# Performance work log

Hardware: AMD Instinct MI355X
Metric: run time of the kernel (lower is better)

## Reference

```python
import jax, jax.numpy as jnp
import numpy as np

N = 500000   # candidates
C = 128      # field centers
D = 64       # latent dim
EPS = 1e-6
TEMP = 0.1
DT = 0.1


def setup_inputs() -> dict:
    key = jax.random.key(0)
    k1, k2, k3, k4 = jax.random.split(key, 4)
    query_z = jax.random.normal(k1, (1, D), dtype=jnp.float32)
    candidate_z = jax.random.normal(k2, (N, D), dtype=jnp.float32)
    centers = jax.random.normal(k3, (C, D), dtype=jnp.float32)
    mus = jax.random.uniform(k4, (C,), dtype=jnp.float32) * 0.5 + 0.1  # positive masses
    return {"query_z": query_z, "candidate_z": candidate_z, "centers": centers, "mus": mus}


def _cdist(a, b):
    # Euclidean distance matrix (|a|^2 + |b|^2 - 2 a.b)^(1/2), clamped for stability
    d2 = (jnp.sum(a * a, axis=-1, keepdims=True)
          + jnp.sum(b * b, axis=-1)[None, :]
          - 2.0 * (a @ b.T))
    return jnp.sqrt(jnp.maximum(d2, 1e-12))


def _potential(z, centers, mus):
    # pot_i = sum_j mu_j / (dist(z_i, c_j) + eps)   -> (len(z),)
    d = _cdist(z, centers)                      # (B, C)
    return jnp.sum(mus[None, :] / (d + EPS), axis=1)


def _pm_field(z, centers, mus):
    # Gravitational flow step: z + dt * sum_j mu_j * (c_j - z) / (r^3 + eps)
    diff = centers[None, :, :] - z[:, None, :]          # (B, C, D)
    r = jnp.sqrt(jnp.maximum(jnp.sum(diff * diff, axis=-1, keepdims=True), 1e-12))
    return z + DT * jnp.sum(mus[None, :, None] * diff / (r ** 3 + EPS), axis=1)


def reference(query_z, candidate_z, centers, mus):
    query_output = _pm_field(query_z, centers, mus)        # (1, D)
    q_pot = _potential(query_z, centers, mus)              # (1,)
    c_pot = _potential(candidate_z, centers, mus)          # (N,)
    logits = -jnp.abs(q_pot - c_pot) / TEMP                # (N,)
    attention = jax.nn.softmax(logits, axis=0)             # (N,)
    return query_output, attention
```

## Files before the change

### kernel.cpp

```cpp
#include <hip/hip_runtime.h>
#include <hip/hip_bf16.h>

#define N_CAND     500000
#define N_PAIRS    15625
#define IT_LOG2E   14.426950408889634f
#define DT_STEP    0.1f
#define POT_BLOCKS 1024
#define STRIDE     (POT_BLOCKS * 4)

typedef __attribute__((ext_vector_type(8))) short  short8;
typedef __attribute__((ext_vector_type(4))) float  floatx4;
typedef __attribute__((ext_vector_type(4))) unsigned int uintx4;

__device__ inline unsigned pk(float lo, float hi) {
    return __builtin_amdgcn_perm(__builtin_bit_cast(unsigned, hi),
                                 __builtin_bit_cast(unsigned, lo), 0x07060302u);
}

__device__ inline short8 pack8(floatx4 v0, floatx4 v1, float& ss) {
    uintx4 w;
    w[0] = pk(v0[0], v0[1]); w[1] = pk(v0[2], v0[3]);
    w[2] = pk(v1[0], v1[1]); w[3] = pk(v1[2], v1[3]);
#pragma unroll
    for (int k = 0; k < 4; ++k) {
        ss = fmaf(v0[k], v0[k], ss);
        ss = fmaf(v1[k], v1[k], ss);
    }
    return __builtin_bit_cast(short8, w);
}

__global__ __attribute__((amdgpu_waves_per_eu(2, 4))) __launch_bounds__(256)
void pot_kernel(const float* __restrict__ qz, const float* __restrict__ cand,
                const float* __restrict__ centers, const float* __restrict__ mus,
                float* __restrict__ out, float* __restrict__ partials) {
    __shared__ __align__(16) short8  cfrag[18][2][64];
    __shared__ __align__(16) floatx4 ncin[8][4];
    __shared__ __align__(16) floatx4 muv8[8][4];
    __shared__ float qred[4], sred[4], wj[128];

    int tid = threadIdx.x, wid = tid >> 6, lane = tid & 63;
    int lr = lane & 15;
    int lg = lane >> 4;

    {
        int j = tid >> 1;
        int h = tid & 1;
        const float* crow = centers + j * 64 + h * 32;
        const float* qrow = qz + h * 32;
        float ssd = 0.f;
#pragma unroll
        for (int k = 0; k < 8; ++k) {
            floatx4 c4 = *(const floatx4*)(crow + k * 4);
            floatx4 q4 = *(const floatx4*)(qrow + k * 4);
#pragma unroll
            for (int x = 0; x < 4; ++x) { float df = c4[x] - q4[x]; ssd = fmaf(df, df, ssd); }
        }
        ssd += __shfl_xor(ssd, 1);
        float rs = __builtin_amdgcn_rsqf(fmaxf(ssd, 1e-12f));
        float mu_j = mus[j];
        float potj = (h == 0) ? mu_j * rs : 0.f;
        if (blockIdx.x == 0 && h == 0)
            wj[j] = mu_j * rs * rs * rs;
#pragma unroll
        for (int m = 1; m < 64; m <<= 1) potj += __shfl_xor(potj, m);
        if (lane == 0) qred[wid] = potj;
    }

#pragma unroll
    for (int c2 = 0; c2 < 2; ++c2) {
        int ct = wid * 2 + c2;
        int j = ct * 16 + lr;
        const float* p = centers + j * 64 + lg * 8;
        float ncp = 0.f;
        short8 b0 = pack8(*(const floatx4*)p,        *(const floatx4*)(p + 4),  ncp);
        short8 b1 = pack8(*(const floatx4*)(p + 32), *(const floatx4*)(p + 36), ncp);
        cfrag[ct][0][lane] = b0;
        cfrag[ct][1][lane] = b1;
        ncp += __shfl_xor(ncp, 16);
        ncp += __shfl_xor(ncp, 32);
        if (lg == 0) ((float*)ncin)[ct * 16 + lr] = -0.5f * ncp;
        if (lg == 1) ((float*)muv8)[ct * 16 + lr] = mus[j];
    }
    __syncthreads();
    float q_pot = qred[0] + qred[1] + qred[2] + qred[3];

    if (blockIdx.x == 0 && tid < 64) {
        float qd = qz[tid];
        float acc = 0.f;
        for (int jj = 0; jj < 128; ++jj)
            acc = fmaf(wj[jj], centers[jj * 64 + tid] - qd, acc);
        out[tid] = fmaf(DT_STEP, acc, qd);
    }

    float lsum = 0.f;
    const float* baseA = cand + (size_t)lr * 64 + lg * 8;
    floatx4 v0, v1, v2, v3, v4, v5, v6, v7;
#define LOADP(pp) { const float* pa = baseA + (size_t)(pp) * 2048;          \
        v0 = *(const floatx4*)pa;        v1 = *(const floatx4*)(pa + 4);    \
        v2 = *(const floatx4*)(pa + 32); v3 = *(const floatx4*)(pa + 36);   \
        const float* pb = pa + 1024;                                        \
        v4 = *(const floatx4*)pb;        v5 = *(const floatx4*)(pb + 4);    \
        v6 = *(const floatx4*)(pb + 32); v7 = *(const floatx4*)(pb + 36); }

    int p = blockIdx.x * 4 + wid;
    LOADP(p);
    while (p < N_PAIRS) {
        float nzA = 0.f, nzB = 0.f;
        short8 afA0 = pack8(v0, v1, nzA), afA1 = pack8(v2, v3, nzA);
        short8 afB0 = pack8(v4, v5, nzB), afB1 = pack8(v6, v7, nzB);
        size_t r0 = (size_t)p * 32;
        p += STRIDE;
        if (p < N_PAIRS) LOADP(p);

        nzA += __shfl_xor(nzA, 16); nzA += __shfl_xor(nzA, 32);
        nzB += __shfl_xor(nzB, 16); nzB += __shfl_xor(nzB, 32);

        float potA = 0.f, potB = 0.f;
#pragma unroll
        for (int ct = 0; ct < 8; ++ct) {
            floatx4 nci = ncin[ct][lg];
            floatx4 m4  = muv8[ct][lg];
            short8 f0 = cfrag[ct][0][lane];
            short8 f1 = cfrag[ct][1][lane];
            floatx4 aA = __builtin_amdgcn_mfma_f32_16x16x32_bf16(f0, afA0, nci, 0, 0, 0);
            aA         = __builtin_amdgcn_mfma_f32_16x16x32_bf16(f1, afA1, aA,  0, 0, 0);
            floatx4 aB = __builtin_amdgcn_mfma_f32_16x16x32_bf16(f0, afB0, nci, 0, 0, 0);
            aB         = __builtin_amdgcn_mfma_f32_16x16x32_bf16(f1, afB1, aB,  0, 0, 0);
#pragma unroll
            for (int r = 0; r < 4; ++r) {
                potA = fmaf(m4[r], __builtin_amdgcn_rsqf(fmaf(-2.f, aA[r], nzA)), potA);
                potB = fmaf(m4[r], __builtin_amdgcn_rsqf(fmaf(-2.f, aB[r], nzB)), potB);
            }
        }
        potA += __shfl_xor(potA, 16); potA += __shfl_xor(potA, 32);
        potB += __shfl_xor(potB, 16); potB += __shfl_xor(potB, 32);

        if (lg == 0) {
            float eA = exp2f(-IT_LOG2E * fabsf(q_pot - potA));
            float eB = exp2f(-IT_LOG2E * fabsf(q_pot - potB));
            out[64 + r0 + lr]      = eA;
            out[64 + r0 + 16 + lr] = eB;
            lsum += eA + eB;
        }
    }
#undef LOADP

#pragma unroll
    for (int m = 1; m < 64; m <<= 1) lsum += __shfl_xor(lsum, m);
    if (lane == 0) sred[wid] = lsum;
    __syncthreads();
    if (tid == 0) partials[blockIdx.x] = sred[0] + sred[1] + sred[2] + sred[3];
}

__global__ __launch_bounds__(256)
void norm_kernel(float* __restrict__ att, const float* __restrict__ partials) {
    int tid = threadIdx.x;
    float p = partials[tid] + partials[tid + 256] + partials[tid + 512] + partials[tid + 768];
#pragma unroll
    for (int m = 1; m < 64; m <<= 1) p += __shfl_xor(p, m);
    __shared__ float red[4];
    if ((tid & 63) == 0) red[tid >> 6] = p;
    __syncthreads();
    float inv = 1.0f / (red[0] + red[1] + red[2] + red[3]);
    int i = blockIdx.x * 256 + tid;
    if (i < N_CAND / 4) {
        floatx4 v = *(floatx4*)(att + (size_t)i * 4);
#pragma unroll
        for (int k = 0; k < 4; ++k) v[k] *= inv;
        *(floatx4*)(att + (size_t)i * 4) = v;
    }
}

extern "C" void kernel_launch(void* const* d_in, const int* in_sizes, int n_in,
                              void* d_out, int out_size, void* d_ws, size_t ws_size,
                              hipStream_t stream) {
    const float* qz   = (const float*)d_in[0];
    const float* cand = (const float*)d_in[1];
    const float* ctr  = (const float*)d_in[2];
    const float* mus  = (const float*)d_in[3];
    float* out = (float*)d_out;
    float* ws  = (float*)d_ws;

    pot_kernel<<<POT_BLOCKS, 256, 0, stream>>>(qz, cand, ctr, mus, out, ws + 256);
    int blocks2 = (N_CAND / 4 + 255) / 256;
    norm_kernel<<<blocks2, 256, 0, stream>>>(out + 64, ws + 256);
}
```

Baseline: 39.84 us.

## Raise occupancy target, drop manual prefetch, hoist center constants into registers

Raises the waves-per-EU minimum from 2 to 3 and removes the software double-buffered candidate prefetch, relying on extra resident waves to hide global load latency instead. The per-center-tile bias and mass vectors now live in registers rather than being re-read from LDS on every iteration. The exp/store epilogue is split across two lane groups so each lane handles one value instead of one group doing both. The main risk is register pressure from the 64 hoisted floats against the tighter VGPR budget, which could cause spills or fail to reach the extra occupancy, and losing the explicit prefetch may expose load latency.

Result: slower. 53.90 us (+35.3%).

```diff
diff --git a/kernel.cpp b/kernel.cpp
--- a/kernel.cpp
+++ b/kernel.cpp
@@ -29,7 +29,7 @@
     return __builtin_bit_cast(short8, w);
 }
 
-__global__ __attribute__((amdgpu_waves_per_eu(2, 4))) __launch_bounds__(256)
+__global__ __attribute__((amdgpu_waves_per_eu(3, 4))) __launch_bounds__(256)
 void pot_kernel(const float* __restrict__ qz, const float* __restrict__ cand,
                 const float* __restrict__ centers, const float* __restrict__ mus,
                 float* __restrict__ out, float* __restrict__ partials) {
@@ -92,58 +92,55 @@
         out[tid] = fmaf(DT_STEP, acc, qd);
     }
 
+    floatx4 ncr[8], mur[8];
+#pragma unroll
+    for (int ct = 0; ct < 8; ++ct) { ncr[ct] = ncin[ct][lg]; mur[ct] = muv8[ct][lg]; }
+
     float lsum = 0.f;
     const float* baseA = cand + (size_t)lr * 64 + lg * 8;
-    floatx4 v0, v1, v2, v3, v4, v5, v6, v7;
-#define LOADP(pp) { const float* pa = baseA + (size_t)(pp) * 2048;          \
-        v0 = *(const floatx4*)pa;        v1 = *(const floatx4*)(pa + 4);    \
-        v2 = *(const floatx4*)(pa + 32); v3 = *(const floatx4*)(pa + 36);   \
-        const float* pb = pa + 1024;                                        \
-        v4 = *(const floatx4*)pb;        v5 = *(const floatx4*)(pb + 4);    \
-        v6 = *(const floatx4*)(pb + 32); v7 = *(const floatx4*)(pb + 36); }
+    for (int p = blockIdx.x * 4 + wid; p < N_PAIRS; p += STRIDE) {
+        const float* pa = baseA + (size_t)p * 2048;
+        floatx4 v0 = *(const floatx4*)pa;
+        floatx4 v1 = *(const floatx4*)(pa + 4);
+        floatx4 v2 = *(const floatx4*)(pa + 32);
+        floatx4 v3 = *(const floatx4*)(pa + 36);
+        const float* pb = pa + 1024;
+        floatx4 v4 = *(const floatx4*)pb;
+        floatx4 v5 = *(const floatx4*)(pb + 4);
+        floatx4 v6 = *(const floatx4*)(pb + 32);
+        floatx4 v7 = *(const floatx4*)(pb + 36);
 
-    int p = blockIdx.x * 4 + wid;
-    LOADP(p);
-    while (p < N_PAIRS) {
         float nzA = 0.f, nzB = 0.f;
         short8 afA0 = pack8(v0, v1, nzA), afA1 = pack8(v2, v3, nzA);
         short8 afB0 = pack8(v4, v5, nzB), afB1 = pack8(v6, v7, nzB);
-        size_t r0 = (size_t)p * 32;
-        p += STRIDE;
-        if (p < N_PAIRS) LOADP(p);
-
         nzA += __shfl_xor(nzA, 16); nzA += __shfl_xor(nzA, 32);
         nzB += __shfl_xor(nzB, 16); nzB += __shfl_xor(nzB, 32);
 
         float potA = 0.f, potB = 0.f;
 #pragma unroll
         for (int ct = 0; ct < 8; ++ct) {
-            floatx4 nci = ncin[ct][lg];
-            floatx4 m4  = muv8[ct][lg];
             short8 f0 = cfrag[ct][0][lane];
             short8 f1 = cfrag[ct][1][lane];
-            floatx4 aA = __builtin_amdgcn_mfma_f32_16x16x32_bf16(f0, afA0, nci, 0, 0, 0);
-            aA         = __builtin_amdgcn_mfma_f32_16x16x32_bf16(f1, afA1, aA,  0, 0, 0);
-            floatx4 aB = __builtin_amdgcn_mfma_f32_16x16x32_bf16(f0, afB0, nci, 0, 0, 0);
-            aB         = __builtin_amdgcn_mfma_f32_16x16x32_bf16(f1, afB1, aB,  0, 0, 0);
+            floatx4 aA = __builtin_amdgcn_mfma_f32_16x16x32_bf16(f0, afA0, ncr[ct], 0, 0, 0);
+            aA         = __builtin_amdgcn_mfma_f32_16x16x32_bf16(f1, afA1, aA,      0, 0, 0);
+            floatx4 aB = __builtin_amdgcn_mfma_f32_16x16x32_bf16(f0, afB0, ncr[ct], 0, 0, 0);
+            aB         = __builtin_amdgcn_mfma_f32_16x16x32_bf16(f1, afB1, aB,      0, 0, 0);
 #pragma unroll
             for (int r = 0; r < 4; ++r) {
-                potA = fmaf(m4[r], __builtin_amdgcn_rsqf(fmaf(-2.f, aA[r], nzA)), potA);
-                potB = fmaf(m4[r], __builtin_amdgcn_rsqf(fmaf(-2.f, aB[r], nzB)), potB);
+                potA = fmaf(mur[ct][r], __builtin_amdgcn_rsqf(fmaf(-2.f, aA[r], nzA)), potA);
+                potB = fmaf(mur[ct][r], __builtin_amdgcn_rsqf(fmaf(-2.f, aB[r], nzB)), potB);
             }
         }
         potA += __shfl_xor(potA, 16); potA += __shfl_xor(potA, 32);
         potB += __shfl_xor(potB, 16); potB += __shfl_xor(potB, 32);
 
-        if (lg == 0) {
-            float eA = exp2f(-IT_LOG2E * fabsf(q_pot - potA));
-            float eB = exp2f(-IT_LOG2E * fabsf(q_pot - potB));
-            out[64 + r0 + lr]      = eA;
-            out[64 + r0 + 16 + lr] = eB;
-            lsum += eA + eB;
+        if (lg < 2) {
+            float pt = (lg == 0) ? potA : potB;
+            float e = exp2f(-IT_LOG2E * fabsf(q_pot - pt));
+            out[64 + (size_t)p * 32 + lg * 16 + lr] = e;
+            lsum += e;
         }
     }
-#undef LOADP
 
 #pragma unroll
     for (int m = 1; m < 64; m <<= 1) lsum += __shfl_xor(lsum, m);
```
